# Optimization experiments

Hardware: AMD Instinct MI355X
Metric: run time of the kernel (lower is better)

## Reference

```python
import jax, jax.numpy as jnp
import numpy as np

B, N, F_IN, T = 16, 512, 32, 24
K, C_OUT = 3, 64


def setup_inputs() -> dict:
    key = jax.random.key(0)
    k1, k2, k3, k4 = jax.random.split(key, 4)
    X = jax.random.normal(k1, (B, N, F_IN, T), dtype=jnp.float32)
    s_a = jax.random.uniform(k2, (B, N, N), dtype=jnp.float32)
    cheb = jax.random.normal(k3, (K, N, N), dtype=jnp.float32)
    # Theta per nn.Parameter(K, c_in, c_out), kaiming-style scale
    Theta = jax.random.normal(k4, (K, F_IN, C_OUT), dtype=jnp.float32) * np.float32(np.sqrt(2.0 / F_IN))
    return {"X": X, "s_a": s_a, "cheb": cheb, "Theta": Theta}


def reference(X, s_a, cheb, Theta):
    # A[k,b,n,m] = T_k[n,m] * s_a[b,n,m]  (attention-masked Chebyshev polynomial)
    A = cheb[:, None, :, :] * s_a[None, :, :, :]  # [K,B,N,N]
    # torch: rhs = bmm(A.permute(0,2,1), X_t); out_t = sum_k rhs @ Theta_k
    # -> out[t,b,m,o] = sum_{k,n,f} A[k,b,n,m] * X[b,n,f,t] * Theta[k,f,o]
    out = jnp.einsum('kbnm,bnft,kfo->tbmo', A, X, Theta)  # [T,B,N,c_out]
    return jax.nn.relu(out)  # graph_conv_act_func == 'relu'
```

## Files before the change

### kernel.cpp

```cpp
#include <hip/hip_runtime.h>
#include <hip/hip_bf16.h>

#define B_ 16
#define N_ 512
#define F_ 32
#define T_ 24
#define K_ 3
#define C_ 64
#define FT_ 768
#define KF_ 96

typedef __attribute__((ext_vector_type(8))) short bf16x8;
typedef __attribute__((ext_vector_type(4))) float f32x4;

static __device__ __forceinline__ ushort f2b(float x) {
  uint u = __float_as_uint(x);
  return (ushort)((u + 0x7fffu + ((u >> 16) & 1u)) >> 16);
}
static __device__ __forceinline__ uint pk2(float a, float b) {
  return (uint)f2b(a) | ((uint)f2b(b) << 16);
}

#define GLOAD_LDS16(g, l)                                                     \
  __builtin_amdgcn_global_load_lds(                                           \
      (const __attribute__((address_space(1))) void*)(g),                     \
      (__attribute__((address_space(3))) void*)(l), 16, 0, 0)

#define XP_PAD 260
__global__ __launch_bounds__(256) void prep(const float* __restrict__ X,
                                            const float* __restrict__ SA,
                                            const float* __restrict__ CH,
                                            ushort* __restrict__ Xt2,
                                            ushort* __restrict__ At) {
  __shared__ ushort L[32 * XP_PAD];
  const int bid = blockIdx.x;
  const int tid = threadIdx.x;
  if (bid < 768) {
    const int local = bid % 48;
    const int b = bid / 48;
    const int n0 = (local & 15) * 32;
    const int fg = local >> 4;
    const float* Xp = X + ((size_t)b * N_ + n0) * FT_ + fg * 8;
#pragma unroll
    for (int it = 0; it < 8; ++it) {
      int c = tid + it * 256;
      int row = c >> 6, rem = c & 63;
      int f = rem >> 1, half = rem & 1;
      float4 v = *(const float4*)(Xp + (size_t)row * FT_ + f * 24 + half * 4);
      uint2 p; p.x = pk2(v.x, v.y); p.y = pk2(v.z, v.w);
      *(uint2*)&L[row * XP_PAD + f * 8 + half * 4] = p;
    }
    __syncthreads();
    const int ft2 = fg * 256 + tid;
    const int f = tid & 31, dt = tid >> 5;
    ushort a[32];
#pragma unroll
    for (int r = 0; r < 32; ++r) a[r] = L[r * XP_PAD + f * 8 + dt];
    uint w[16];
#pragma unroll
    for (int q = 0; q < 16; ++q) w[q] = (uint)a[2 * q] | ((uint)a[2 * q + 1] << 16);
    ushort* op = Xt2 + ((size_t)b * FT_ + ft2) * N_ + n0;
#pragma unroll
    for (int q = 0; q < 4; ++q) {
      uint4 v; v.x = w[4*q]; v.y = w[4*q+1]; v.z = w[4*q+2]; v.w = w[4*q+3];
      *((uint4*)op + q) = v;
    }
  } else {
    const int a = bid - 768;
    const int kb = a >> 4;
    const int k = kb >> 4, b = kb & 15;
    const int sub = a & 15;
    const int ml = (tid & 15) * 4, nl = (tid >> 4) * 4;
#pragma unroll
    for (int c = 0; c < 4; ++c) {
      const int tile = sub * 4 + c;
      const int m0 = (tile & 7) * 64, n0 = (tile >> 3) * 64;
      const float* cp = CH + ((size_t)k * N_ + n0 + nl) * N_ + m0 + ml;
      const float* sp = SA + ((size_t)b * N_ + n0 + nl) * N_ + m0 + ml;
      float4 p[4];
#pragma unroll
      for (int q = 0; q < 4; ++q) {
        float4 cv = *(const float4*)(cp + (size_t)q * N_);
        float4 sv = *(const float4*)(sp + (size_t)q * N_);
        p[q] = make_float4(cv.x * sv.x, cv.y * sv.y, cv.z * sv.z, cv.w * sv.w);
      }
      ushort* ob = At + (size_t)kb * N_ * N_ + (size_t)(m0 + ml) * N_ + n0 + nl;
#pragma unroll
      for (int s = 0; s < 4; ++s) {
        uint2 w;
        w.x = pk2(((const float*)&p[0])[s], ((const float*)&p[1])[s]);
        w.y = pk2(((const float*)&p[2])[s], ((const float*)&p[3])[s]);
        *(uint2*)(ob + (size_t)s * N_) = w;
      }
    }
  }
}

__global__ __launch_bounds__(256, 3) void stage1(const ushort* __restrict__ Xt2,
                                                 const ushort* __restrict__ At,
                                                 ushort* __restrict__ R2) {
  __shared__ __align__(16) ushort Abuf[128 * 64];
  __shared__ __align__(16) ushort Bbuf[3][64 * 64];

  const int bid = blockIdx.x;
  const int logical = (bid & 7) * 96 + (bid >> 3);
  const int b = logical / 48;
  const int tile = logical % 48;
  const int ft0 = (tile >> 3) * 128;
  const int m0 = (tile & 7) * 64;
  const int tid = threadIdx.x, lane = tid & 63, wid = tid >> 6;
  const int wft = (wid >> 1) * 64, wm = (wid & 1) * 32;
  const int srow = lane >> 3;
  const int scolS = ((lane & 7) * 16) ^ (srow << 4);

  const char* Xbase = (const char*)(Xt2 + ((size_t)b * FT_ + ft0) * N_);
  const char* Bk[3];
#pragma unroll
  for (int kq = 0; kq < 3; ++kq)
    Bk[kq] = (const char*)(At + ((size_t)(kq * 16 + b) * N_ + m0) * N_);

  f32x4 acc[3][4][2];
#pragma unroll
  for (int kq = 0; kq < 3; ++kq)
#pragma unroll
    for (int i = 0; i < 4; ++i)
#pragma unroll
      for (int j = 0; j < 2; ++j) acc[kq][i][j] = (f32x4){0.f, 0.f, 0.f, 0.f};

  for (int nb = 0; nb < 8; ++nb) {
    __syncthreads();
#pragma unroll
    for (int c = 0; c < 4; ++c) {
      const int s = wid * 4 + c;
      const size_t go = (size_t)(s * 8 + srow) * 1024 + nb * 128 + scolS;
      GLOAD_LDS16(Xbase + go, (char*)Abuf + s * 1024);
    }
#pragma unroll
    for (int c = 0; c < 6; ++c) {
      const int idx = wid * 6 + c;
      const int kq = idx >> 3, seg = idx & 7;
      const size_t go = (size_t)(seg * 8 + srow) * 1024 + nb * 128 + scolS;
      GLOAD_LDS16(Bk[kq] + go, (char*)Bbuf[kq] + seg * 1024);
    }
    __syncthreads();
#pragma unroll
    for (int kk = 0; kk < 2; ++kk) {
      const int cb = (kk * 64 + (lane >> 4) * 16) ^ ((lane & 7) << 4);
      bf16x8 af[4];
#pragma unroll
      for (int i = 0; i < 4; ++i)
        af[i] = *(const bf16x8*)((const char*)Abuf + (wft + i * 16 + (lane & 15)) * 128 + cb);
#pragma unroll
      for (int kq = 0; kq < 3; ++kq) {
        bf16x8 bf[2];
#pragma unroll
        for (int j = 0; j < 2; ++j)
          bf[j] = *(const bf16x8*)((const char*)Bbuf[kq] + (wm + j * 16 + (lane & 15)) * 128 + cb);
#pragma unroll
        for (int i = 0; i < 4; ++i)
#pragma unroll
          for (int j = 0; j < 2; ++j)
            acc[kq][i][j] = __builtin_amdgcn_mfma_f32_16x16x32_bf16(af[i], bf[j], acc[kq][i][j], 0, 0, 0);
      }
    }
  }

  const int col = lane & 15, rg4 = (lane >> 4) * 4;
#pragma unroll
  for (int kq = 0; kq < 3; ++kq)
#pragma unroll
    for (int i = 0; i < 4; ++i) {
      const int ft2 = ft0 + wft + i * 16 + rg4;
      const int t = ft2 >> 5, f = ft2 & 31;
      const size_t rowbase = ((size_t)(b * T_ + t) * 12 + kq * 4 + (f >> 3)) * 4096 + (f & 7);
#pragma unroll
      for (int j = 0; j < 2; ++j) {
        const int m = m0 + wm + j * 16 + col;
        uint2 w;
        w.x = pk2(acc[kq][i][j][0], acc[kq][i][j][1]);
        w.y = pk2(acc[kq][i][j][2], acc[kq][i][j][3]);
        *(uint2*)(R2 + rowbase + (size_t)m * 8) = w;
      }
    }
}

__global__ __launch_bounds__(256, 2) void stage2(const ushort* __restrict__ R2,
                                                 const float* __restrict__ TH,
                                                 float* __restrict__ Out) {
  const int mh = blockIdx.x;
  const int t = blockIdx.y, b = blockIdx.z;
  const int tid = threadIdx.x, lane = tid & 63, wid = tid >> 6;
  const int m0w = mh * 256 + wid * 64;
  const int col = lane & 15, g = lane >> 4, rg4 = g * 4;

  bf16x8 bfr[3][4];
#pragma unroll
  for (int ks = 0; ks < 3; ++ks)
#pragma unroll
    for (int j = 0; j < 4; ++j) {
      const float* tp = TH + (size_t)(ks * 32 + g * 8) * C_ + j * 16 + col;
      bf16x8 v;
#pragma unroll
      for (int q = 0; q < 8; ++q) v[q] = (short)f2b(tp[(size_t)q * C_]);
      bfr[ks][j] = v;
    }

  const ushort* Rb = R2 + ((size_t)(b * T_ + t) * 12) * 4096;
  float* Ob = Out + ((size_t)t * B_ + b) * N_ * C_;

#pragma unroll
  for (int i = 0; i < 4; ++i) {
    const int m = m0w + i * 16;
    bf16x8 af[3];
#pragma unroll
    for (int ks = 0; ks < 3; ++ks)
      af[ks] = *(const bf16x8*)(Rb + (size_t)(ks * 4 + g) * 4096 + (size_t)(m + col) * 8);
    f32x4 acc[4];
#pragma unroll
    for (int j = 0; j < 4; ++j) acc[j] = (f32x4){0.f, 0.f, 0.f, 0.f};
#pragma unroll
    for (int ks = 0; ks < 3; ++ks)
#pragma unroll
      for (int j = 0; j < 4; ++j)
        acc[j] = __builtin_amdgcn_mfma_f32_16x16x32_bf16(af[ks], bfr[ks][j], acc[j], 0, 0, 0);
#pragma unroll
    for (int j = 0; j < 4; ++j)
#pragma unroll
      for (int r = 0; r < 4; ++r)
        Ob[(size_t)(m + rg4 + r) * C_ + j * 16 + col] = fmaxf(acc[j][r], 0.f);
  }
}

extern "C" void kernel_launch(void* const* d_in, const int* in_sizes, int n_in,
                              void* d_out, int out_size, void* d_ws, size_t ws_size,
                              hipStream_t stream) {
  const float* X  = (const float*)d_in[0];
  const float* SA = (const float*)d_in[1];
  const float* CH = (const float*)d_in[2];
  const float* TH = (const float*)d_in[3];
  float* Out = (float*)d_out;

  char* ws = (char*)d_ws;
  ushort* R2  = (ushort*)(ws);
  ushort* Xt2 = (ushort*)(ws + 37748736);
  ushort* At  = (ushort*)(ws + 37748736 + 12582912);

  prep<<<dim3(1536), 256, 0, stream>>>(X, SA, CH, Xt2, At);
  stage1<<<dim3(768), 256, 0, stream>>>(Xt2, At, R2);
  stage2<<<dim3(2, 24, 16), 256, 0, stream>>>(R2, TH, Out);
}
```

Measured before the change: 145.5 us.

## Fuse Theta contraction and ReLU into stage1 epilogue, removing R2 round-trip

Stage1 now writes its bf16 intermediate (A^T X per k) into shared memory instead of a global R2 buffer. Each block then multiplies it by a pre-transposed bf16 Theta with MFMA and writes the ReLU output directly. The prep kernel gains one extra block that converts and transposes Theta. This removes the separate stage2 launch and the global write and read of the large intermediate. In exchange it adds shared-memory reuse, extra syncs and more register pressure in stage1.

New measurement: 135.7 us. 6.7% less time.

```diff
diff --git a/kernel.cpp b/kernel.cpp
--- a/kernel.cpp
+++ b/kernel.cpp
@@ -9,6 +9,7 @@
 #define C_ 64
 #define FT_ 768
 #define KF_ 96
+#define KFP 104
 
 typedef __attribute__((ext_vector_type(8))) short bf16x8;
 typedef __attribute__((ext_vector_type(4))) float f32x4;
@@ -30,8 +31,10 @@
 __global__ __launch_bounds__(256) void prep(const float* __restrict__ X,
                                             const float* __restrict__ SA,
                                             const float* __restrict__ CH,
+                                            const float* __restrict__ TH,
                                             ushort* __restrict__ Xt2,
-                                            ushort* __restrict__ At) {
+                                            ushort* __restrict__ At,
+                                            ushort* __restrict__ Th2) {
   __shared__ ushort L[32 * XP_PAD];
   const int bid = blockIdx.x;
   const int tid = threadIdx.x;
@@ -65,7 +68,7 @@
       uint4 v; v.x = w[4*q]; v.y = w[4*q+1]; v.z = w[4*q+2]; v.w = w[4*q+3];
       *((uint4*)op + q) = v;
     }
-  } else {
+  } else if (bid < 1536) {
     const int a = bid - 768;
     const int kb = a >> 4;
     const int k = kb >> 4, b = kb & 15;
@@ -93,14 +96,22 @@
         *(uint2*)(ob + (size_t)s * N_) = w;
       }
     }
+  } else {
+    for (int i = tid; i < C_ * KF_; i += 256) {
+      int o = i / KF_, kf = i - o * KF_;
+      Th2[i] = f2b(TH[(size_t)kf * C_ + o]);
+    }
   }
 }
 
 __global__ __launch_bounds__(256, 3) void stage1(const ushort* __restrict__ Xt2,
                                                  const ushort* __restrict__ At,
-                                                 ushort* __restrict__ R2) {
-  __shared__ __align__(16) ushort Abuf[128 * 64];
-  __shared__ __align__(16) ushort Bbuf[3][64 * 64];
+                                                 const ushort* __restrict__ Th2,
+                                                 float* __restrict__ Out) {
+  __shared__ __align__(16) char smem[4 * 64 * KFP * 2];
+  ushort* Abuf = (ushort*)smem;
+  ushort* Bbuf = (ushort*)(smem + 16384);
+  ushort* P    = (ushort*)smem;
 
   const int bid = blockIdx.x;
   const int logical = (bid & 7) * 96 + (bid >> 3);
@@ -140,7 +151,7 @@
       const int idx = wid * 6 + c;
       const int kq = idx >> 3, seg = idx & 7;
       const size_t go = (size_t)(seg * 8 + srow) * 1024 + nb * 128 + scolS;
-      GLOAD_LDS16(Bk[kq] + go, (char*)Bbuf[kq] + seg * 1024);
+      GLOAD_LDS16(Bk[kq] + go, (char*)Bbuf + kq * 8192 + seg * 1024);
     }
     __syncthreads();
 #pragma unroll
@@ -155,7 +166,7 @@
         bf16x8 bf[2];
 #pragma unroll
         for (int j = 0; j < 2; ++j)
-          bf[j] = *(const bf16x8*)((const char*)Bbuf[kq] + (wm + j * 16 + (lane & 15)) * 128 + cb);
+          bf[j] = *(const bf16x8*)((const char*)Bbuf + kq * 8192 + (wm + j * 16 + (lane & 15)) * 128 + cb);
 #pragma unroll
         for (int i = 0; i < 4; ++i)
 #pragma unroll
@@ -165,70 +176,57 @@
     }
   }
 
-  const int col = lane & 15, rg4 = (lane >> 4) * 4;
+  const int col = lane & 15, g = lane >> 4, rg4 = g * 4;
+  __syncthreads();
 #pragma unroll
   for (int kq = 0; kq < 3; ++kq)
 #pragma unroll
     for (int i = 0; i < 4; ++i) {
-      const int ft2 = ft0 + wft + i * 16 + rg4;
-      const int t = ft2 >> 5, f = ft2 & 31;
-      const size_t rowbase = ((size_t)(b * T_ + t) * 12 + kq * 4 + (f >> 3)) * 4096 + (f & 7);
+      const int ftl = wft + i * 16 + rg4;
+      const int tl = ftl >> 5, f0 = ftl & 31;
 #pragma unroll
       for (int j = 0; j < 2; ++j) {
-        const int m = m0 + wm + j * 16 + col;
+        const int m = wm + j * 16 + col;
         uint2 w;
         w.x = pk2(acc[kq][i][j][0], acc[kq][i][j][1]);
         w.y = pk2(acc[kq][i][j][2], acc[kq][i][j][3]);
-        *(uint2*)(R2 + rowbase + (size_t)m * 8) = w;
-      }
-    }
-}
-
-__global__ __launch_bounds__(256, 2) void stage2(const ushort* __restrict__ R2,
-                                                 const float* __restrict__ TH,
-                                                 float* __restrict__ Out) {
-  const int mh = blockIdx.x;
-  const int t = blockIdx.y, b = blockIdx.z;
-  const int tid = threadIdx.x, lane = tid & 63, wid = tid >> 6;
-  const int m0w = mh * 256 + wid * 64;
-  const int col = lane & 15, g = lane >> 4, rg4 = g * 4;
-
-  bf16x8 bfr[3][4];
-#pragma unroll
-  for (int ks = 0; ks < 3; ++ks)
-#pragma unroll
-    for (int j = 0; j < 4; ++j) {
-      const float* tp = TH + (size_t)(ks * 32 + g * 8) * C_ + j * 16 + col;
-      bf16x8 v;
-#pragma unroll
-      for (int q = 0; q < 8; ++q) v[q] = (short)f2b(tp[(size_t)q * C_]);
-      bfr[ks][j] = v;
-    }
-
-  const ushort* Rb = R2 + ((size_t)(b * T_ + t) * 12) * 4096;
-  float* Ob = Out + ((size_t)t * B_ + b) * N_ * C_;
-
-#pragma unroll
-  for (int i = 0; i < 4; ++i) {
-    const int m = m0w + i * 16;
-    bf16x8 af[3];
-#pragma unroll
-    for (int ks = 0; ks < 3; ++ks)
-      af[ks] = *(const bf16x8*)(Rb + (size_t)(ks * 4 + g) * 4096 + (size_t)(m + col) * 8);
-    f32x4 acc[4];
-#pragma unroll
-    for (int j = 0; j < 4; ++j) acc[j] = (f32x4){0.f, 0.f, 0.f, 0.f};
-#pragma unroll
-    for (int ks = 0; ks < 3; ++ks)
-#pragma unroll
-      for (int j = 0; j < 4; ++j)
-        acc[j] = __builtin_amdgcn_mfma_f32_16x16x32_bf16(af[ks], bfr[ks][j], acc[j], 0, 0, 0);
-#pragma unroll
-    for (int j = 0; j < 4; ++j)
+        *(uint2*)&P[(size_t)(tl * 64 + m) * KFP + kq * 32 + f0] = w;
+      }
+    }
+  __syncthreads();
+
+  bf16x8 bq[3][4];
+#pragma unroll
+  for (int kc = 0; kc < 3; ++kc)
+#pragma unroll
+    for (int j2 = 0; j2 < 4; ++j2)
+      bq[kc][j2] = *(const bf16x8*)(Th2 + (size_t)(j2 * 16 + col) * KF_ + kc * 32 + g * 8);
+
+  f32x4 acc2[4][4];
+#pragma unroll
+  for (int i2 = 0; i2 < 4; ++i2)
+#pragma unroll
+    for (int j2 = 0; j2 < 4; ++j2) acc2[i2][j2] = (f32x4){0.f, 0.f, 0.f, 0.f};
+
+#pragma unroll
+  for (int kc = 0; kc < 3; ++kc)
+#pragma unroll
+    for (int i2 = 0; i2 < 4; ++i2) {
+      const bf16x8 a2 = *(const bf16x8*)&P[(size_t)(wid * 64 + i2 * 16 + col) * KFP + kc * 32 + g * 8];
+#pragma unroll
+      for (int j2 = 0; j2 < 4; ++j2)
+        acc2[i2][j2] = __builtin_amdgcn_mfma_f32_16x16x32_bf16(a2, bq[kc][j2], acc2[i2][j2], 0, 0, 0);
+    }
+
+  const int t = (tile >> 3) * 4 + wid;
+  float* Ob = Out + ((size_t)(t * B_ + b) * N_ + m0) * C_;
+#pragma unroll
+  for (int i2 = 0; i2 < 4; ++i2)
+#pragma unroll
+    for (int j2 = 0; j2 < 4; ++j2)
 #pragma unroll
       for (int r = 0; r < 4; ++r)
-        Ob[(size_t)(m + rg4 + r) * C_ + j * 16 + col] = fmaxf(acc[j][r], 0.f);
-  }
+        Ob[(size_t)(i2 * 16 + rg4 + r) * C_ + j2 * 16 + col] = fmaxf(acc2[i2][j2][r], 0.f);
 }
 
 extern "C" void kernel_launch(void* const* d_in, const int* in_sizes, int n_in,
@@ -241,11 +239,10 @@
   float* Out = (float*)d_out;
 
   char* ws = (char*)d_ws;
-  ushort* R2  = (ushort*)(ws);
-  ushort* Xt2 = (ushort*)(ws + 37748736);
-  ushort* At  = (ushort*)(ws + 37748736 + 12582912);
-
-  prep<<<dim3(1536), 256, 0, stream>>>(X, SA, CH, Xt2, At);
-  stage1<<<dim3(768), 256, 0, stream>>>(Xt2, At, R2);
-  stage2<<<dim3(2, 24, 16), 256, 0, stream>>>(R2, TH, Out);
-}
+  ushort* Xt2 = (ushort*)(ws);
+  ushort* At  = (ushort*)(ws + 12582912);
+  ushort* Th2 = (ushort*)(ws + 12582912 + 25165824);
+
+  prep<<<dim3(1537), 256, 0, stream>>>(X, SA, CH, TH, Xt2, At, Th2);
+  stage1<<<dim3(768), 256, 0, stream>>>(Xt2, At, Th2, Out);
+}
```
